# Kernel optimization log

Hardware: AMD Instinct MI355X
Metric: run time of the kernel (lower is better)

The kernel has to match this reference:

```python
import jax, jax.numpy as jnp
import numpy as np
from jax import lax

B, EMB, CIN, COUT, K, H, W = 16, 768, 64, 64, 3, 112, 112
HID = EMB // 4  # reduction_ratio=4
TOTAL = COUT * CIN * K * K


def setup_inputs() -> dict:
    key = jax.random.key(0)
    k1, k2, k3, k4 = jax.random.split(key, 4)
    cls_token = jax.random.normal(k1, (B, 1, EMB), dtype=jnp.float32)
    features = jax.random.normal(k2, (B, CIN, H, W), dtype=jnp.float32)
    W1 = jax.random.normal(k3, (EMB, HID), dtype=jnp.float32) * 0.02
    b1 = jnp.zeros((HID,), dtype=jnp.float32)
    W2 = jax.random.normal(k4, (HID, TOTAL), dtype=jnp.float32) * 0.01
    b2 = jnp.zeros((TOTAL,), dtype=jnp.float32)
    return {"cls_token": cls_token, "features": features,
            "W1": W1, "b1": b1, "W2": W2, "b2": b2}


def _per_sample_conv(feat, kern):
    # feat: (CIN, H, W); kern: (COUT, CIN, K, K) -> (COUT, H, W)
    out = lax.conv_general_dilated(
        feat[None], kern, window_strides=(1, 1), padding="SAME",
        dimension_numbers=("NCHW", "OIHW", "NCHW"))
    return out[0]


def reference(cls_token, features, W1, b1, W2, b2):
    # Dynamic kernel generation from CLS token
    x = cls_token[:, 0, :]                      # (B, EMB)
    h = jax.nn.relu(x @ W1 + b1)                # (B, HID)
    params = jnp.tanh(h @ W2 + b2)              # (B, TOTAL)
    kernel = params.reshape(B, COUT, CIN, K, K)
    # Per-sample convolution (equivalent to unfold + bmm in torch)
    conv_feat = jax.vmap(_per_sample_conv)(features, kernel)  # (B, COUT, H, W)
    # in_channels == out_channels -> identity shortcut
    return conv_feat + features
```

## Files before the change

kernel.cpp:

```cpp
#include <hip/hip_runtime.h>
#include <hip/hip_bf16.h>

#define BB   16
#define EMB  768
#define CIN  64
#define COUT 64
#define HH   112
#define WW   112
#define HID  192
#define TOTAL 36864
#define KSZ  576
#define PW   114
#define CELL 128
#define ROWB (PW * CELL)
#define RING 6

typedef short bf16x8 __attribute__((ext_vector_type(8)));
typedef float f32x4  __attribute__((ext_vector_type(4)));
typedef int   i32x4  __attribute__((ext_vector_type(4)));

static __device__ __forceinline__ unsigned short f2bf(float f) {
    unsigned u = __float_as_uint(f);
    u += 0x7FFF + ((u >> 16) & 1);
    return (unsigned short)(u >> 16);
}

static __device__ __forceinline__ bf16x8 pack8(const float* v) {
    bf16x8 r;
    #pragma unroll
    for (int j = 0; j < 8; ++j) r[j] = (short)f2bf(v[j]);
    return r;
}

#define GLOAD_LDS16(g, l) \
    __builtin_amdgcn_global_load_lds((const __attribute__((address_space(1))) void*)(g), \
                                     (__attribute__((address_space(3))) void*)(l), 16, 0, 0)

#define WAIT_VMCNT(n) do { asm volatile("s_waitcnt vmcnt(" #n ")" ::: "memory"); \
                           __builtin_amdgcn_sched_barrier(0); } while (0)

__global__ __launch_bounds__(256) void pre_mlp1(const float* __restrict__ feat,
                                                unsigned short* __restrict__ P,
                                                const float* __restrict__ cls,
                                                const float* __restrict__ W1,
                                                const float* __restrict__ b1,
                                                float* __restrict__ h) {
    __shared__ float smem[EMB + 16 * 17];
    const int bid = blockIdx.x;
    const int tid = threadIdx.x;

    if (bid < HH * BB) {
        const int b = bid & 15;
        const int y = bid >> 4;
        unsigned short* Prow = P + ((size_t)b * PW + y + 1) * (PW * 64);
        if (tid < 16) {
            const int cell = (tid >> 3) ? (PW - 1) : 0;
            *(i32x4*)((char*)Prow + cell * CELL + (tid & 7) * 16) = (i32x4){0, 0, 0, 0};
        }
        const int o = tid >> 5;
        const int q = tid & 31;
        if (q < 28) {
            const float* fb = feat + (((size_t)b * CIN + o * 8) * HH + y) * WW + 4 * q;
            f32x4 v[8];
            #pragma unroll
            for (int j = 0; j < 8; ++j) v[j] = *(const f32x4*)(fb + (size_t)j * (HH * WW));
            #pragma unroll
            for (int i = 0; i < 4; ++i) {
                unsigned short w[8];
                #pragma unroll
                for (int j = 0; j < 8; ++j) w[j] = f2bf(v[j][i]);
                *(bf16x8*)(Prow + (size_t)(4 * q + i + 1) * 64 + o * 8) = *(bf16x8*)w;
            }
        }
    } else if (bid < HH * BB + 32) {
        const int idx = bid - HH * BB;
        const int b = idx & 15;
        unsigned short* Prow = P + ((size_t)b * PW + ((idx >> 4) ? (PW - 1) : 0)) * (PW * 64);
        #pragma unroll
        for (int k = 0; k < 4; ++k) {
            const int i = tid + 256 * k;
            if (i < 912) ((i32x4*)Prow)[i] = (i32x4){0, 0, 0, 0};
        }
    } else {
        float* xs  = smem;
        float* red = smem + EMB;
        const int idx = bid - (HH * BB + 32);
        const int b   = idx / 12;
        const int jg  = idx - 12 * b;
        for (int i = tid; i < EMB; i += 256) xs[i] = cls[b * EMB + i];
        __syncthreads();
        const int j16 = tid & 15;
        const int kq  = tid >> 4;
        const int j   = jg * 16 + j16;
        float acc = 0.f;
        #pragma unroll
        for (int k = kq * 48; k < kq * 48 + 48; ++k) acc += xs[k] * W1[k * HID + j];
        red[j16 * 17 + kq] = acc;
        __syncthreads();
        if (tid < 16) {
            float s = b1[jg * 16 + tid];
            #pragma unroll
            for (int q = 0; q < 16; ++q) s += red[tid * 17 + q];
            h[b * HID + jg * 16 + tid] = fmaxf(s, 0.f);
        }
    }
}

__global__ __launch_bounds__(256) void mlp2_kernel(const float* __restrict__ h,
                                                   const float* __restrict__ W2,
                                                   const float* __restrict__ b2,
                                                   unsigned short* __restrict__ Ag) {
    __shared__ float hs[16 * 193];
    const int tid = threadIdx.x;
    for (int i = tid; i < BB * HID; i += 256) {
        const int bb = i / HID;
        hs[bb * 193 + (i - bb * HID)] = h[i];
    }
    __syncthreads();
    const int wave = tid >> 6;
    const int lane = tid & 63;
    const int lg   = lane >> 4;
    const int ln   = lane & 15;
    const int t0   = (blockIdx.x * 4 + wave) * 16;

    bf16x8 a6[6];
    #pragma unroll
    for (int kk = 0; kk < 6; ++kk) {
        float v[8];
        #pragma unroll
        for (int j = 0; j < 8; ++j) v[j] = hs[ln * 193 + kk * 32 + lg * 8 + j];
        a6[kk] = pack8(v);
    }

    f32x4 acc = (f32x4){0.f, 0.f, 0.f, 0.f};
    #pragma unroll
    for (int kk = 0; kk < 6; ++kk) {
        float w[8];
        #pragma unroll
        for (int j = 0; j < 8; ++j)
            w[j] = W2[(size_t)(kk * 32 + lg * 8 + j) * TOTAL + t0 + ln];
        acc = __builtin_amdgcn_mfma_f32_16x16x32_bf16(a6[kk], pack8(w), acc, 0, 0, 0);
    }

    const int t    = t0 + ln;
    const float bias = b2[t];
    const int co  = t / KSZ;
    const int rem = t - co * KSZ;
    const int ci  = rem / 9;
    const int p9  = rem - ci * 9;
    const float idv = (p9 == 4 && co == ci) ? 1.f : 0.f;
    unsigned short* pA = Ag + (size_t)(p9 * 64 + co) * 64 + ci;
    #pragma unroll
    for (int rg = 0; rg < 4; ++rg) {
        const int bi = lg * 4 + rg;
        pA[(size_t)bi * TOTAL] = f2bf(tanhf(acc[rg] + bias) + idv);
    }
}

__global__ __launch_bounds__(256, 1) void conv_kernel(const unsigned short* __restrict__ Ag,
                                                      const unsigned short* __restrict__ P,
                                                      float* __restrict__ out) {
    extern __shared__ __align__(16) char lds[];
    const int tid = threadIdx.x;
    const int bid   = (blockIdx.x & 7) * 28 + (blockIdx.x >> 3);
    const int b     = bid / 14;
    const int strip = bid - b * 14;
    const int Y0    = strip * 8;

    const int wave = tid >> 6;
    const int lane = tid & 63;
    const int cog  = wave & 1;
    const int r    = wave >> 1;
    const int lg   = lane >> 4;
    const int ln   = lane & 15;

    const unsigned short* Ab = Ag + (size_t)b * 9 * 4096;
    bf16x8 af[9][2][2];
    #pragma unroll
    for (int p9 = 0; p9 < 9; ++p9)
        #pragma unroll
        for (int ct = 0; ct < 2; ++ct)
            #pragma unroll
            for (int cib = 0; cib < 2; ++cib)
                af[p9][ct][cib] = *(const bf16x8*)(Ab + (size_t)(p9 * 64 + cog * 32 + ct * 16 + ln) * 64
                                                   + cib * 32 + lg * 8);

    const char* Pb = (const char*)P + ((size_t)b * PW + Y0) * ROWB;

    if (tid < 228) {
        #pragma unroll
        for (int k = 0; k < 16; ++k) {
            const int i = k * 228 + tid;
            const int s = i / 912, jj = i - s * 912;
            const int c = jj >> 3, g = jj & 7;
            GLOAD_LDS16(Pb + (size_t)s * ROWB + c * CELL + ((g ^ (c & 7)) << 4),
                        lds + (size_t)i * 16);
        }
    }
    WAIT_VMCNT(0);
    __builtin_amdgcn_s_barrier();
    __builtin_amdgcn_sched_barrier(0);

    #pragma unroll
    for (int t = 0; t < 4; ++t) {
        if (t > 0) {
            WAIT_VMCNT(56);
            __builtin_amdgcn_s_barrier();
            __builtin_amdgcn_sched_barrier(0);
        }
        if (t < 3) {
            const int lr0 = 2 * t + 4;
            const int s0  = lr0 % RING;
            const char* Ps = Pb + (size_t)lr0 * ROWB;
            char* ldst = lds + (size_t)s0 * ROWB;
            if (tid < 228) {
                #pragma unroll
                for (int k = 0; k < 8; ++k) {
                    const int i = k * 228 + tid;
                    const int s = i / 912, jj = i - s * 912;
                    const int c = jj >> 3, g = jj & 7;
                    GLOAD_LDS16(Ps + (size_t)s * ROWB + c * CELL + ((g ^ (c & 7)) << 4),
                                ldst + (size_t)i * 16);
                }
            }
        }

        const char* rp[3];
        #pragma unroll
        for (int kh = 0; kh < 3; ++kh) {
            const int lr = 2 * t + r + kh;
            const int sl = lr - (lr >= RING ? RING : 0);
            rp[kh] = lds + (size_t)sl * ROWB;
        }

        f32x4 acc[2][7];
        #pragma unroll
        for (int ct = 0; ct < 2; ++ct)
            #pragma unroll
            for (int tt = 0; tt < 7; ++tt) acc[ct][tt] = (f32x4){0.f, 0.f, 0.f, 0.f};

        #pragma unroll
        for (int p9 = 0; p9 < 9; ++p9) {
            const int kh = p9 / 3, kw = p9 - 3 * kh;
            const char* lbase = rp[kh] + (ln + kw) * CELL;
            const int   c7    = (ln + kw) & 7;
            #pragma unroll
            for (int cib = 0; cib < 2; ++cib) {
                const int sw = ((cib * 4 + lg) ^ c7) << 4;
                #pragma unroll
                for (int tt = 0; tt < 7; ++tt) {
                    const bf16x8 bf = *(const bf16x8*)(lbase + tt * (16 * CELL) + sw);
                    acc[0][tt] = __builtin_amdgcn_mfma_f32_16x16x32_bf16(af[p9][0][cib], bf, acc[0][tt], 0, 0, 0);
                    acc[1][tt] = __builtin_amdgcn_mfma_f32_16x16x32_bf16(af[p9][1][cib], bf, acc[1][tt], 0, 0, 0);
                }
            }
        }

        const int y = Y0 + 2 * t + r;
        float* ob = out + (((size_t)b * COUT + cog * 32 + lg * 4) * HH + y) * WW + ln;
        #pragma unroll
        for (int ct = 0; ct < 2; ++ct)
            #pragma unroll
            for (int tt = 0; tt < 7; ++tt)
                #pragma unroll
                for (int rg = 0; rg < 4; ++rg)
                    ob[((size_t)(ct * 16 + rg)) * HH * WW + tt * 16] = acc[ct][tt][rg];
    }
}

extern "C" void kernel_launch(void* const* d_in, const int* in_sizes, int n_in,
                              void* d_out, int out_size, void* d_ws, size_t ws_size,
                              hipStream_t stream) {
    const float* cls      = (const float*)d_in[0];
    const float* features = (const float*)d_in[1];
    const float* W1       = (const float*)d_in[2];
    const float* b1       = (const float*)d_in[3];
    const float* W2       = (const float*)d_in[4];
    const float* b2       = (const float*)d_in[5];
    float* out = (float*)d_out;

    float*          h  = (float*)d_ws;
    unsigned short* Ag = (unsigned short*)(h + BB * HID);
    unsigned short* P  = Ag + (size_t)BB * 9 * 4096;

    (void)hipFuncSetAttribute((const void*)conv_kernel,
                              hipFuncAttributeMaxDynamicSharedMemorySize, RING * ROWB);

    pre_mlp1<<<HH * BB + 32 + 192, 256, 0, stream>>>(features, P, cls, W1, b1, h);
    mlp2_kernel<<<TOTAL / 64, 256, 0, stream>>>(h, W2, b2, Ag);
    conv_kernel<<<224, 256, RING * ROWB, stream>>>(Ag, P, out);
}
```

Before: 59.76 us.

## Regroup launches: run MLP1 alone, fuse feature packing with MLP2, add nontemporal hints

Moves the small MLP1 into its own launch and merges the feature-to-bf16 padded packing with the MLP2 kernel-generation work in one grid. The larger MLP2 can then overlap with the bandwidth-heavy repacking instead of running serialized after it. It also remaps packing block indices across batches, and adds nontemporal loads for features and W2 and nontemporal stores for the conv output to reduce cache pollution. The launch count stays at three, and the fused kernel's blocks need more LDS for the h staging, which may affect occupancy.

```diff
diff --git a/kernel.cpp b/kernel.cpp
--- a/kernel.cpp
+++ b/kernel.cpp
@@ -39,19 +39,47 @@
 #define WAIT_VMCNT(n) do { asm volatile("s_waitcnt vmcnt(" #n ")" ::: "memory"); \
                            __builtin_amdgcn_sched_barrier(0); } while (0)
 
-__global__ __launch_bounds__(256) void pre_mlp1(const float* __restrict__ feat,
+__global__ __launch_bounds__(256) void mlp1_kernel(const float* __restrict__ cls,
+                                                   const float* __restrict__ W1,
+                                                   const float* __restrict__ b1,
+                                                   float* __restrict__ h) {
+    __shared__ float xs[EMB];
+    __shared__ float red[16][17];
+    const int b   = blockIdx.x / 12;
+    const int jg  = blockIdx.x - 12 * b;
+    const int tid = threadIdx.x;
+    for (int i = tid; i < EMB; i += 256) xs[i] = cls[b * EMB + i];
+    __syncthreads();
+    const int j16 = tid & 15;
+    const int kq  = tid >> 4;
+    const int j   = jg * 16 + j16;
+    float acc = 0.f;
+    #pragma unroll
+    for (int k = kq * 48; k < kq * 48 + 48; ++k) acc += xs[k] * W1[k * HID + j];
+    red[j16][kq] = acc;
+    __syncthreads();
+    if (tid < 16) {
+        float s = b1[jg * 16 + tid];
+        #pragma unroll
+        for (int q = 0; q < 16; ++q) s += red[tid][q];
+        h[b * HID + jg * 16 + tid] = fmaxf(s, 0.f);
+    }
+}
+
+__global__ __launch_bounds__(256) void pre_mlp2(const float* __restrict__ feat,
                                                 unsigned short* __restrict__ P,
-                                                const float* __restrict__ cls,
-                                                const float* __restrict__ W1,
-                                                const float* __restrict__ b1,
-                                                float* __restrict__ h) {
-    __shared__ float smem[EMB + 16 * 17];
+                                                const float* __restrict__ h,
+                                                const float* __restrict__ W2,
+                                                const float* __restrict__ b2,
+                                                unsigned short* __restrict__ Ag) {
+    __shared__ float hs[16 * 193];
     const int bid = blockIdx.x;
     const int tid = threadIdx.x;
 
     if (bid < HH * BB) {
-        const int b = bid & 15;
-        const int y = bid >> 4;
+        const int j = bid >> 3;
+        const int b = (bid & 7) * 2 + (j >= 112 ? 1 : 0);
+        const int y = j - (j >= 112 ? 112 : 0);
         unsigned short* Prow = P + ((size_t)b * PW + y + 1) * (PW * 64);
         if (tid < 16) {
             const int cell = (tid >> 3) ? (PW - 1) : 0;
@@ -63,18 +91,19 @@
             const float* fb = feat + (((size_t)b * CIN + o * 8) * HH + y) * WW + 4 * q;
             f32x4 v[8];
             #pragma unroll
-            for (int j = 0; j < 8; ++j) v[j] = *(const f32x4*)(fb + (size_t)j * (HH * WW));
+            for (int j2 = 0; j2 < 8; ++j2)
+                v[j2] = __builtin_nontemporal_load((const f32x4*)(fb + (size_t)j2 * (HH * WW)));
             #pragma unroll
             for (int i = 0; i < 4; ++i) {
                 unsigned short w[8];
                 #pragma unroll
-                for (int j = 0; j < 8; ++j) w[j] = f2bf(v[j][i]);
+                for (int j2 = 0; j2 < 8; ++j2) w[j2] = f2bf(v[j2][i]);
                 *(bf16x8*)(Prow + (size_t)(4 * q + i + 1) * 64 + o * 8) = *(bf16x8*)w;
             }
         }
     } else if (bid < HH * BB + 32) {
         const int idx = bid - HH * BB;
-        const int b = idx & 15;
+        const int b   = idx & 15;
         unsigned short* Prow = P + ((size_t)b * PW + ((idx >> 4) ? (PW - 1) : 0)) * (PW * 64);
         #pragma unroll
         for (int k = 0; k < 4; ++k) {
@@ -82,78 +111,50 @@
             if (i < 912) ((i32x4*)Prow)[i] = (i32x4){0, 0, 0, 0};
         }
     } else {
-        float* xs  = smem;
-        float* red = smem + EMB;
-        const int idx = bid - (HH * BB + 32);
-        const int b   = idx / 12;
-        const int jg  = idx - 12 * b;
-        for (int i = tid; i < EMB; i += 256) xs[i] = cls[b * EMB + i];
+        const int blk = bid - (HH * BB + 32);
+        for (int i = tid; i < BB * HID; i += 256) {
+            const int bb = i / HID;
+            hs[bb * 193 + (i - bb * HID)] = h[i];
+        }
         __syncthreads();
-        const int j16 = tid & 15;
-        const int kq  = tid >> 4;
-        const int j   = jg * 16 + j16;
-        float acc = 0.f;
-        #pragma unroll
-        for (int k = kq * 48; k < kq * 48 + 48; ++k) acc += xs[k] * W1[k * HID + j];
-        red[j16 * 17 + kq] = acc;
-        __syncthreads();
-        if (tid < 16) {
-            float s = b1[jg * 16 + tid];
-            #pragma unroll
-            for (int q = 0; q < 16; ++q) s += red[tid * 17 + q];
-            h[b * HID + jg * 16 + tid] = fmaxf(s, 0.f);
-        }
-    }
-}
-
-__global__ __launch_bounds__(256) void mlp2_kernel(const float* __restrict__ h,
-                                                   const float* __restrict__ W2,
-                                                   const float* __restrict__ b2,
-                                                   unsigned short* __restrict__ Ag) {
-    __shared__ float hs[16 * 193];
-    const int tid = threadIdx.x;
-    for (int i = tid; i < BB * HID; i += 256) {
-        const int bb = i / HID;
-        hs[bb * 193 + (i - bb * HID)] = h[i];
-    }
-    __syncthreads();
-    const int wave = tid >> 6;
-    const int lane = tid & 63;
-    const int lg   = lane >> 4;
-    const int ln   = lane & 15;
-    const int t0   = (blockIdx.x * 4 + wave) * 16;
-
-    bf16x8 a6[6];
-    #pragma unroll
-    for (int kk = 0; kk < 6; ++kk) {
-        float v[8];
-        #pragma unroll
-        for (int j = 0; j < 8; ++j) v[j] = hs[ln * 193 + kk * 32 + lg * 8 + j];
-        a6[kk] = pack8(v);
-    }
-
-    f32x4 acc = (f32x4){0.f, 0.f, 0.f, 0.f};
-    #pragma unroll
-    for (int kk = 0; kk < 6; ++kk) {
-        float w[8];
-        #pragma unroll
-        for (int j = 0; j < 8; ++j)
-            w[j] = W2[(size_t)(kk * 32 + lg * 8 + j) * TOTAL + t0 + ln];
-        acc = __builtin_amdgcn_mfma_f32_16x16x32_bf16(a6[kk], pack8(w), acc, 0, 0, 0);
-    }
-
-    const int t    = t0 + ln;
-    const float bias = b2[t];
-    const int co  = t / KSZ;
-    const int rem = t - co * KSZ;
-    const int ci  = rem / 9;
-    const int p9  = rem - ci * 9;
-    const float idv = (p9 == 4 && co == ci) ? 1.f : 0.f;
-    unsigned short* pA = Ag + (size_t)(p9 * 64 + co) * 64 + ci;
-    #pragma unroll
-    for (int rg = 0; rg < 4; ++rg) {
-        const int bi = lg * 4 + rg;
-        pA[(size_t)bi * TOTAL] = f2bf(tanhf(acc[rg] + bias) + idv);
+        const int wave = tid >> 6;
+        const int lane = tid & 63;
+        const int lg   = lane >> 4;
+        const int ln   = lane & 15;
+        const int t0   = (blk * 4 + wave) * 16;
+
+        bf16x8 a6[6];
+        #pragma unroll
+        for (int kk = 0; kk < 6; ++kk) {
+            float v[8];
+            #pragma unroll
+            for (int j = 0; j < 8; ++j) v[j] = hs[ln * 193 + kk * 32 + lg * 8 + j];
+            a6[kk] = pack8(v);
+        }
+
+        f32x4 acc = (f32x4){0.f, 0.f, 0.f, 0.f};
+        #pragma unroll
+        for (int kk = 0; kk < 6; ++kk) {
+            float w[8];
+            #pragma unroll
+            for (int j = 0; j < 8; ++j)
+                w[j] = __builtin_nontemporal_load(W2 + (size_t)(kk * 32 + lg * 8 + j) * TOTAL + t0 + ln);
+            acc = __builtin_amdgcn_mfma_f32_16x16x32_bf16(a6[kk], pack8(w), acc, 0, 0, 0);
+        }
+
+        const int t    = t0 + ln;
+        const float bias = b2[t];
+        const int co  = t / KSZ;
+        const int rem = t - co * KSZ;
+        const int ci  = rem / 9;
+        const int p9  = rem - ci * 9;
+        const float idv = (p9 == 4 && co == ci) ? 1.f : 0.f;
+        unsigned short* pA = Ag + (size_t)(p9 * 64 + co) * 64 + ci;
+        #pragma unroll
+        for (int rg = 0; rg < 4; ++rg) {
+            const int bi = lg * 4 + rg;
+            pA[(size_t)bi * TOTAL] = f2bf(tanhf(acc[rg] + bias) + idv);
+        }
     }
 }
 
@@ -264,7 +265,8 @@
             for (int tt = 0; tt < 7; ++tt)
                 #pragma unroll
                 for (int rg = 0; rg < 4; ++rg)
-                    ob[((size_t)(ct * 16 + rg)) * HH * WW + tt * 16] = acc[ct][tt][rg];
+                    __builtin_nontemporal_store(acc[ct][tt][rg],
+                        ob + ((size_t)(ct * 16 + rg)) * HH * WW + tt * 16);
     }
 }
 
@@ -286,7 +288,7 @@
     (void)hipFuncSetAttribute((const void*)conv_kernel,
                               hipFuncAttributeMaxDynamicSharedMemorySize, RING * ROWB);
 
-    pre_mlp1<<<HH * BB + 32 + 192, 256, 0, stream>>>(features, P, cls, W1, b1, h);
-    mlp2_kernel<<<TOTAL / 64, 256, 0, stream>>>(h, W2, b2, Ag);
+    mlp1_kernel<<<192, 256, 0, stream>>>(cls, W1, b1, h);
+    pre_mlp2<<<HH * BB + 32 + 576, 256, 0, stream>>>(features, P, h, W2, b2, Ag);
     conv_kernel<<<224, 256, RING * ROWB, stream>>>(Ag, P, out);
 }
```

Result: slower. 67.22 us (+12.5%).
